# Optimization experiments

Measured on AMD Instinct MI355X. Metric: run time of the kernel, lower is better.

## Reference

```python
import jax, jax.numpy as jnp
import numpy as np

N_HEADS = 16
ROPE_BASE = 10000.0


def _rope_tables(T, head_dim):
    inv_freq = 1.0 / (ROPE_BASE ** (jnp.arange(0, head_dim, 2, dtype=jnp.float32) / head_dim))
    freqs = jnp.outer(jnp.arange(T, dtype=jnp.float32), inv_freq)  # (T, head_dim/2)
    emb = jnp.concatenate([freqs, freqs], axis=-1)  # (T, head_dim)
    return jnp.cos(emb), jnp.sin(emb)


def _rotate_half(u):
    u1, u2 = jnp.split(u, 2, axis=-1)
    return jnp.concatenate([-u2, u1], axis=-1)


def setup_inputs() -> dict:
    key = jax.random.key(0)
    k1, k2, k3 = jax.random.split(key, 3)
    B, T, D = 2, 2048, 1024
    x = jax.random.normal(k1, (B, T, D), dtype=jnp.float32)
    W_qkv = jax.random.normal(k2, (D, 3 * D), dtype=jnp.float32) * (1.0 / np.sqrt(D))
    W_out = jax.random.normal(k3, (D, D), dtype=jnp.float32) * (1.0 / np.sqrt(D))
    return {"x": x, "W_qkv": W_qkv, "W_out": W_out}


def reference(x, W_qkv, W_out):
    B, T, D = x.shape
    H = N_HEADS
    Dh = D // H
    # fused QKV projection
    qkv = (x @ W_qkv).reshape(B, T, 3, H, Dh)
    q = jnp.transpose(qkv[:, :, 0], (0, 2, 1, 3))  # (B,H,T,Dh)
    k = jnp.transpose(qkv[:, :, 1], (0, 2, 1, 3))
    v = jnp.transpose(qkv[:, :, 2], (0, 2, 1, 3))
    # RoPE
    cos, sin = _rope_tables(T, Dh)  # (T, Dh), broadcasts over (B,H)
    q = q * cos + _rotate_half(q) * sin
    k = k * cos + _rotate_half(k) * sin
    # causal SDPA
    scale = 1.0 / jnp.sqrt(jnp.asarray(Dh, dtype=x.dtype))
    scores = jnp.einsum('bhqd,bhkd->bhqk', q, k) * scale
    causal = jnp.tril(jnp.ones((T, T), dtype=bool))
    scores = jnp.where(causal, scores, jnp.asarray(-jnp.inf, dtype=scores.dtype))
    attn = jax.nn.softmax(scores, axis=-1)
    out = jnp.einsum('bhqk,bhkd->bhqd', attn, v)
    out = jnp.transpose(out, (0, 2, 1, 3)).reshape(B, T, D)
    return out @ W_out
```

## Files before the change

### kernel.cpp

```cpp
#include <hip/hip_runtime.h>
#include <math.h>

typedef unsigned short u16;
typedef short bf16x8 __attribute__((ext_vector_type(8)));
typedef float f32x4 __attribute__((ext_vector_type(4)));

#define ROPE_SC 0.18033688011112042f

__device__ __forceinline__ u16 f2bf(float f) {
    union { float f; unsigned u; } x; x.f = f;
    unsigned u = x.u;
    unsigned r = (u + 0x7fffu + ((u >> 16) & 1u)) >> 16;
    return (u16)r;
}
__device__ __forceinline__ unsigned pack2(float a, float b) {
    return (unsigned)f2bf(a) | ((unsigned)f2bf(b) << 16);
}
__device__ __forceinline__ f32x4 mfma16(bf16x8 a, bf16x8 b, f32x4 c) {
    return __builtin_amdgcn_mfma_f32_16x16x32_bf16(a, b, c, 0, 0, 0);
}
__device__ __forceinline__ void gload_lds16(const void* g, void* l) {
    __builtin_amdgcn_global_load_lds((const __attribute__((address_space(1))) void*)g,
                                     (__attribute__((address_space(3))) void*)l,
                                     16, 0, 0);
}

__global__ void cvt_bf16(const float* __restrict__ X, u16* __restrict__ Y) {
    int i = (blockIdx.x * 256 + threadIdx.x) * 4;
    float4 v = *(const float4*)(X + i);
    uint2 o;
    o.x = pack2(v.x, v.y);
    o.y = pack2(v.z, v.w);
    *(uint2*)(Y + i) = o;
}

__global__ void transpose_cvt(const float* __restrict__ W, u16* __restrict__ Wt,
                              int R, int C) {
    __shared__ u16 tile[32][33];
    int tx = threadIdx.x & 31, ty = threadIdx.x >> 5;
    int bx = blockIdx.x * 32;
    int by = blockIdx.y * 32;
#pragma unroll
    for (int r = ty; r < 32; r += 8)
        tile[r][tx] = f2bf(W[(size_t)(by + r) * C + bx + tx]);
    __syncthreads();
#pragma unroll
    for (int r = ty; r < 32; r += 8)
        Wt[(size_t)(bx + r) * R + by + tx] = tile[tx][r];
}

__global__ void rope_tab(float* __restrict__ tab) {
    int i = blockIdx.x * 256 + threadIdx.x;
    int t = i >> 5, d = i & 31;
    float invf = powf(10000.0f, -(float)d / 32.0f);
    float ang = (float)t * invf;
    tab[i] = cosf(ang);
    tab[i + 65536] = sinf(ang);
}

__global__ __launch_bounds__(256) void gemm_qkv(const u16* __restrict__ A,
                                                const u16* __restrict__ Bt,
                                                const float* __restrict__ tab,
                                                u16* __restrict__ qb,
                                                u16* __restrict__ kb,
                                                u16* __restrict__ vt,
                                                int M, int N, int K) {
    __shared__ u16 lA[128 * 64];
    __shared__ u16 lB[128 * 64];
    const int tid = threadIdx.x;
    const int wave = tid >> 6, lane = tid & 63;
    const int l15 = lane & 15, l4 = lane >> 4;
    const int nwg = gridDim.x * gridDim.y;
    const int orig = blockIdx.y * gridDim.x + blockIdx.x;
    const int swz = (orig & 7) * (nwg >> 3) + (orig >> 3);
    const int m0 = (swz / gridDim.x) * 128, n0 = (swz % gridDim.x) * 128;
    const int wm = (wave >> 1) * 64, wn = (wave & 1) * 64;
    f32x4 acc[4][4] = {};
    for (int k0 = 0; k0 < K; k0 += 64) {
#pragma unroll
        for (int it = 0; it < 4; ++it) {
            int c = it * 256 + wave * 64 + lane;
            int r = c >> 3, s = c & 7;
            int sd = ((s ^ (r & 7)) << 3);
            gload_lds16(A + (size_t)(m0 + r) * K + k0 + sd,
                        &lA[(size_t)(it * 256 + wave * 64) * 8]);
            gload_lds16(Bt + (size_t)(n0 + r) * K + k0 + sd,
                        &lB[(size_t)(it * 256 + wave * 64) * 8]);
        }
        __syncthreads();
#pragma unroll
        for (int kk = 0; kk < 2; ++kk) {
            bf16x8 af[4], bf[4];
#pragma unroll
            for (int mi = 0; mi < 4; ++mi) {
                int row = wm + mi * 16 + l15;
                af[mi] = *(const bf16x8*)(&lA[row * 64 + (((kk * 4 + l4) ^ (row & 7)) << 3)]);
            }
#pragma unroll
            for (int ni = 0; ni < 4; ++ni) {
                int row = wn + ni * 16 + l15;
                bf[ni] = *(const bf16x8*)(&lB[row * 64 + (((kk * 4 + l4) ^ (row & 7)) << 3)]);
            }
#pragma unroll
            for (int mi = 0; mi < 4; ++mi)
#pragma unroll
                for (int ni = 0; ni < 4; ++ni)
                    acc[mi][ni] = mfma16(af[mi], bf[ni], acc[mi][ni]);
        }
        __syncthreads();
    }
    const int colg = n0 + wn;
    const int region = colg >> 10;
    const int h = (colg & 1023) >> 6;
    if (region == 2) {
#pragma unroll
        for (int mi = 0; mi < 4; ++mi) {
            int t0 = m0 + wm + mi * 16 + l4 * 4;
            int b = t0 >> 11, tq0 = t0 & 2047;
#pragma unroll
            for (int ni = 0; ni < 4; ++ni) {
                int dcol = ni * 16 + l15;
                uint2 pk;
                pk.x = pack2(acc[mi][ni][0], acc[mi][ni][1]);
                pk.y = pack2(acc[mi][ni][2], acc[mi][ni][3]);
                *(uint2*)(vt + ((size_t)(b * 16 + h) * 64 + dcol) * 2048 + tq0) = pk;
            }
        }
    } else {
        const float sc = (region == 0) ? ROPE_SC : 1.0f;
        u16* dst = (region == 0) ? qb : kb;
#pragma unroll
        for (int mi = 0; mi < 4; ++mi)
#pragma unroll
            for (int i = 0; i < 4; ++i) {
                int t = m0 + wm + mi * 16 + l4 * 4 + i;
                int b = t >> 11, tq = t & 2047;
                const float* tcb = tab + tq * 32;
                const float* tsb = tab + 65536 + tq * 32;
                size_t base = ((size_t)(b * 16 + h) * 2048 + tq) * 64;
#pragma unroll
                for (int ni = 0; ni < 2; ++ni) {
                    int d32 = ni * 16 + l15;
                    float cs = tcb[d32], sn = tsb[d32];
                    float a = acc[mi][ni][i], bb = acc[mi][ni + 2][i];
                    dst[base + d32]      = f2bf((a * cs - bb * sn) * sc);
                    dst[base + d32 + 32] = f2bf((bb * cs + a * sn) * sc);
                }
            }
    }
}

__global__ __launch_bounds__(256) void gemm_bt_n64(const u16* __restrict__ A,
                                                   const u16* __restrict__ Bt,
                                                   float* __restrict__ C,
                                                   int M, int N, int K) {
    __shared__ u16 lA[128 * 64];
    __shared__ u16 lB[64 * 64];
    const int tid = threadIdx.x;
    const int wave = tid >> 6, lane = tid & 63;
    const int l15 = lane & 15, l4 = lane >> 4;
    const int nwg = gridDim.x * gridDim.y;
    const int orig = blockIdx.y * gridDim.x + blockIdx.x;
    const int swz = (orig & 7) * (nwg >> 3) + (orig >> 3);
    const int m0 = (swz / gridDim.x) * 128, n0 = (swz % gridDim.x) * 64;
    const int wm = (wave >> 1) * 64, wn = (wave & 1) * 32;
    f32x4 acc[4][2] = {};
    for (int k0 = 0; k0 < K; k0 += 64) {
#pragma unroll
        for (int it = 0; it < 4; ++it) {
            int c = it * 256 + wave * 64 + lane;
            int r = c >> 3, s = c & 7;
            int sd = ((s ^ (r & 7)) << 3);
            gload_lds16(A + (size_t)(m0 + r) * K + k0 + sd,
                        &lA[(size_t)(it * 256 + wave * 64) * 8]);
        }
#pragma unroll
        for (int it = 0; it < 2; ++it) {
            int c = it * 256 + wave * 64 + lane;
            int r = c >> 3, s = c & 7;
            int sd = ((s ^ (r & 7)) << 3);
            gload_lds16(Bt + (size_t)(n0 + r) * K + k0 + sd,
                        &lB[(size_t)(it * 256 + wave * 64) * 8]);
        }
        __syncthreads();
#pragma unroll
        for (int kk = 0; kk < 2; ++kk) {
            bf16x8 af[4], bf[2];
#pragma unroll
            for (int mi = 0; mi < 4; ++mi) {
                int row = wm + mi * 16 + l15;
                af[mi] = *(const bf16x8*)(&lA[row * 64 + (((kk * 4 + l4) ^ (row & 7)) << 3)]);
            }
#pragma unroll
            for (int ni = 0; ni < 2; ++ni) {
                int row = wn + ni * 16 + l15;
                bf[ni] = *(const bf16x8*)(&lB[row * 64 + (((kk * 4 + l4) ^ (row & 7)) << 3)]);
            }
#pragma unroll
            for (int mi = 0; mi < 4; ++mi)
#pragma unroll
                for (int ni = 0; ni < 2; ++ni)
                    acc[mi][ni] = mfma16(af[mi], bf[ni], acc[mi][ni]);
        }
        __syncthreads();
    }
#pragma unroll
    for (int mi = 0; mi < 4; ++mi)
#pragma unroll
        for (int ni = 0; ni < 2; ++ni)
#pragma unroll
            for (int i = 0; i < 4; ++i) {
                int r = m0 + wm + mi * 16 + l4 * 4 + i;
                int cc = n0 + wn + ni * 16 + l15;
                C[(size_t)r * N + cc] = acc[mi][ni][i];
            }
}

__global__ __launch_bounds__(256, 2) void flash11(const u16* __restrict__ qb,
                                                  const u16* __restrict__ kb,
                                                  const u16* __restrict__ vt,
                                                  u16* __restrict__ ao) {
    __shared__ u16 lK[2][64 * 64];
    __shared__ u16 lV[2][64 * 64];
    const int orig = blockIdx.x;
    const int xcd = orig & 7, p = orig >> 3;
    const int bh = xcd * 4 + (p & 3);
    const int j = (p < 32) ? ((p >> 2) & 7) : 15 - ((p >> 2) & 7);
    const int b = bh >> 4, h = bh & 15;
    const int tid = threadIdx.x;
    const int wave = tid >> 6, lane = tid & 63;
    const int l15 = lane & 15, l4 = lane >> 4;
    const int niter = 2 * (j + 1);
    const u16* qptr = qb + (size_t)bh * 2048 * 64;
    const u16* kptr = kb + (size_t)bh * 2048 * 64;
    const u16* vptr = vt + (size_t)bh * 64 * 2048;

    int qrow[2];
    bf16x8 q0[2], q1[2];
#pragma unroll
    for (int g = 0; g < 2; ++g) {
        qrow[g] = j * 128 + wave * 32 + g * 16 + l15;
        q0[g] = *(const bf16x8*)(qptr + (size_t)qrow[g] * 64 + l4 * 8);
        q1[g] = *(const bf16x8*)(qptr + (size_t)qrow[g] * 64 + 32 + l4 * 8);
    }

    f32x4 O[2][4] = {};
    float mrun[2] = { -INFINITY, -INFINITY }, lrun[2] = { 0.f, 0.f };

    int idxO[4];
#pragma unroll
    for (int i = 0; i < 4; ++i) idxO[i] = (lane & 48) | (l4 * 4 + i);

    const int r0q = ((l15 >> 2) << 3) | (l15 & 3);

    auto stage = [&](int buf, int kv0) {
#pragma unroll
        for (int it = 0; it < 2; ++it) {
            int cb = wave * 64 + it * 256;
            int c = cb + lane;
            int r = c >> 3, s = c & 7;
            int fK = (r & 3) | ((r >> 1) & 4);
            gload_lds16(kptr + (size_t)(kv0 + r) * 64 + ((s ^ fK) << 3), &lK[buf][cb * 8]);
            gload_lds16(vptr + (size_t)r * 2048 + kv0 + ((s ^ (r & 7)) << 3), &lV[buf][cb * 8]);
        }
    };
    auto ldK = [&](int buf, int row, int slot) -> bf16x8 {
        int f = (row & 3) | ((row >> 1) & 4);
        return *(const bf16x8*)(&lK[buf][row * 64 + ((slot ^ f) << 3)]);
    };
    auto ldV = [&](int buf, int row, int slot) -> bf16x8 {
        return *(const bf16x8*)(&lV[buf][row * 64 + ((slot ^ (row & 7)) << 3)]);
    };

    auto smpack = [&](f32x4 S[4], float& mr, float& lr, f32x4 Ov[4],
                      bf16x8 af[2], bool diag, int kv0, int qr) {
        float p2[4][4];
#pragma unroll
        for (int m = 0; m < 4; ++m)
#pragma unroll
            for (int i = 0; i < 4; ++i) {
                float s = S[m][i];
                if (diag && (kv0 + ((m >> 1) << 5) + (l4 << 3) + ((m & 1) << 2) + i > qr))
                    s = -INFINITY;
                p2[m][i] = s;
            }
        float m = p2[0][0];
#pragma unroll
        for (int c = 0; c < 4; ++c)
#pragma unroll
            for (int i = 0; i < 4; ++i) m = fmaxf(m, p2[c][i]);
        m = fmaxf(m, __shfl_xor(m, 16));
        m = fmaxf(m, __shfl_xor(m, 32));
        float mnew = fmaxf(mr, m);
        float corr = __builtin_amdgcn_exp2f(mr - mnew);
        float rs = 0.f;
#pragma unroll
        for (int c = 0; c < 4; ++c)
#pragma unroll
            for (int i = 0; i < 4; ++i) { p2[c][i] = __builtin_amdgcn_exp2f(p2[c][i] - mnew); rs += p2[c][i]; }
        rs += __shfl_xor(rs, 16);
        rs += __shfl_xor(rs, 32);
        lr = lr * corr + rs;
        mr = mnew;
#pragma unroll
        for (int i = 0; i < 4; ++i) {
            float cf = __shfl(corr, idxO[i]);
#pragma unroll
            for (int c2 = 0; c2 < 4; ++c2) Ov[c2][i] *= cf;
        }
        unsigned w[4][2];
#pragma unroll
        for (int c = 0; c < 4; ++c) {
            asm("v_cvt_pk_bf16_f32 %0, %1, %2" : "=v"(w[c][0]) : "v"(p2[c][0]), "v"(p2[c][1]));
            asm("v_cvt_pk_bf16_f32 %0, %1, %2" : "=v"(w[c][1]) : "v"(p2[c][2]), "v"(p2[c][3]));
        }
#pragma unroll
        for (int ks = 0; ks < 2; ++ks) {
            union { unsigned u[4]; bf16x8 v; } cvt;
            cvt.u[0] = w[2 * ks][0];
            cvt.u[1] = w[2 * ks][1];
            cvt.u[2] = w[2 * ks + 1][0];
            cvt.u[3] = w[2 * ks + 1][1];
            af[ks] = cvt.v;
        }
    };

    stage(0, 0);
    for (int kvb = 0; kvb < niter; ++kvb) {
        const int cur = kvb & 1;
        const int kv0 = kvb * 64;
        if (kvb < niter - 1) {
            stage(cur ^ 1, kv0 + 64);
            asm volatile("s_waitcnt vmcnt(4)" ::: "memory");
        } else {
            asm volatile("s_waitcnt vmcnt(0)" ::: "memory");
        }
        __builtin_amdgcn_s_barrier();
        __builtin_amdgcn_sched_barrier(0);

        f32x4 S0[4] = {}, S1[4] = {};
#pragma unroll
        for (int mm = 0; mm < 4; ++mm) {
            int row = r0q + ((mm >> 1) << 5) + ((mm & 1) << 2);
            bf16x8 kf0 = ldK(cur, row, l4);
            bf16x8 kf1 = ldK(cur, row, 4 + l4);
            S0[mm] = mfma16(kf0, q0[0], S0[mm]);
            S0[mm] = mfma16(kf1, q1[0], S0[mm]);
            S1[mm] = mfma16(kf0, q0[1], S1[mm]);
            S1[mm] = mfma16(kf1, q1[1], S1[mm]);
        }
        const bool diag = (kvb >= niter - 2);
        bf16x8 af0[2], af1[2];
        smpack(S0, mrun[0], lrun[0], O[0], af0, diag, kv0, qrow[0]);
        smpack(S1, mrun[1], lrun[1], O[1], af1, diag, kv0, qrow[1]);
#pragma unroll
        for (int ks = 0; ks < 2; ++ks)
#pragma unroll
            for (int c2 = 0; c2 < 4; ++c2) {
                bf16x8 vf = ldV(cur, c2 * 16 + l15, ks * 4 + l4);
                O[0][c2] = mfma16(af0[ks], vf, O[0][c2]);
                O[1][c2] = mfma16(af1[ks], vf, O[1][c2]);
            }
        __builtin_amdgcn_s_barrier();
    }

#pragma unroll
    for (int g = 0; g < 2; ++g)
#pragma unroll
        for (int i = 0; i < 4; ++i) {
            float lv = __shfl(lrun[g], idxO[i]);
            float rcp = 1.f / lv;
            int qg = j * 128 + wave * 32 + g * 16 + l4 * 4 + i;
#pragma unroll
            for (int c2 = 0; c2 < 4; ++c2)
                ao[(size_t)(b * 2048 + qg) * 1024 + h * 64 + c2 * 16 + l15] = f2bf(O[g][c2][i] * rcp);
        }
}

extern "C" void kernel_launch(void* const* d_in, const int* in_sizes, int n_in,
                              void* d_out, int out_size, void* d_ws, size_t ws_size,
                              hipStream_t stream) {
    const float* x    = (const float*)d_in[0];
    const float* Wqkv = (const float*)d_in[1];
    const float* Wout = (const float*)d_in[2];
    float* out = (float*)d_out;
    char* ws = (char*)d_ws;

    u16*   xb  = (u16*)(ws + 0);
    u16*   Wtq = (u16*)(ws + 8388608);
    u16*   Wto = (u16*)(ws + 14680064);
    u16*   qb  = (u16*)(ws + 67108864);
    u16*   kb  = (u16*)(ws + 75497472);
    u16*   vt  = (u16*)(ws + 83886080);
    float* tab = (float*)(ws + 92274688);
    u16*   ao  = (u16*)(ws + 0);

    cvt_bf16<<<dim3(4096), dim3(256), 0, stream>>>(x, xb);
    transpose_cvt<<<dim3(96, 32), dim3(256), 0, stream>>>(Wqkv, Wtq, 1024, 3072);
    transpose_cvt<<<dim3(32, 32), dim3(256), 0, stream>>>(Wout, Wto, 1024, 1024);
    rope_tab<<<dim3(256), dim3(256), 0, stream>>>(tab);
    gemm_qkv<<<dim3(24, 32), dim3(256), 0, stream>>>(xb, Wtq, tab, qb, kb, vt, 4096, 3072, 1024);
    flash11<<<dim3(512), dim3(256), 0, stream>>>(qb, kb, vt, ao);
    gemm_bt_n64<<<dim3(16, 32), dim3(256), 0, stream>>>(ao, Wto, out, 4096, 1024, 1024);
}
```

Before: 131.3 us.

## Use 8-wave GEMM blocks and 64-row flash tiles with more workgroups

Both GEMMs now launch 512 threads per block, with each wave owning half as many M rows. This raises wave-level parallelism and shrinks per-wave register footprint. The attention kernel goes back to 64-query-row tiles, one 16-row group per wave, and runs 1024 blocks with a new causal pairing schedule across XCDs and occupancy hint 4. The aim is better load balance and latency hiding, at the cost of less K/V reuse per block and more block overhead.

Result: faster. 110.8 us (-15.6%).

```diff
diff --git a/kernel.cpp b/kernel.cpp
--- a/kernel.cpp
+++ b/kernel.cpp
@@ -58,7 +58,7 @@
     tab[i + 65536] = sinf(ang);
 }
 
-__global__ __launch_bounds__(256) void gemm_qkv(const u16* __restrict__ A,
+__global__ __launch_bounds__(512) void gemm_qkv(const u16* __restrict__ A,
                                                 const u16* __restrict__ Bt,
                                                 const float* __restrict__ tab,
                                                 u16* __restrict__ qb,
@@ -74,25 +74,24 @@
     const int orig = blockIdx.y * gridDim.x + blockIdx.x;
     const int swz = (orig & 7) * (nwg >> 3) + (orig >> 3);
     const int m0 = (swz / gridDim.x) * 128, n0 = (swz % gridDim.x) * 128;
-    const int wm = (wave >> 1) * 64, wn = (wave & 1) * 64;
-    f32x4 acc[4][4] = {};
+    const int wm = (wave >> 1) * 32, wn = (wave & 1) * 64;
+    f32x4 acc[2][4] = {};
     for (int k0 = 0; k0 < K; k0 += 64) {
 #pragma unroll
-        for (int it = 0; it < 4; ++it) {
-            int c = it * 256 + wave * 64 + lane;
+        for (int it = 0; it < 2; ++it) {
+            int cb = it * 512 + wave * 64;
+            int c = cb + lane;
             int r = c >> 3, s = c & 7;
             int sd = ((s ^ (r & 7)) << 3);
-            gload_lds16(A + (size_t)(m0 + r) * K + k0 + sd,
-                        &lA[(size_t)(it * 256 + wave * 64) * 8]);
-            gload_lds16(Bt + (size_t)(n0 + r) * K + k0 + sd,
-                        &lB[(size_t)(it * 256 + wave * 64) * 8]);
+            gload_lds16(A + (size_t)(m0 + r) * K + k0 + sd, &lA[(size_t)cb * 8]);
+            gload_lds16(Bt + (size_t)(n0 + r) * K + k0 + sd, &lB[(size_t)cb * 8]);
         }
         __syncthreads();
 #pragma unroll
         for (int kk = 0; kk < 2; ++kk) {
-            bf16x8 af[4], bf[4];
-#pragma unroll
-            for (int mi = 0; mi < 4; ++mi) {
+            bf16x8 af[2], bf[4];
+#pragma unroll
+            for (int mi = 0; mi < 2; ++mi) {
                 int row = wm + mi * 16 + l15;
                 af[mi] = *(const bf16x8*)(&lA[row * 64 + (((kk * 4 + l4) ^ (row & 7)) << 3)]);
             }
@@ -102,7 +101,7 @@
                 bf[ni] = *(const bf16x8*)(&lB[row * 64 + (((kk * 4 + l4) ^ (row & 7)) << 3)]);
             }
 #pragma unroll
-            for (int mi = 0; mi < 4; ++mi)
+            for (int mi = 0; mi < 2; ++mi)
 #pragma unroll
                 for (int ni = 0; ni < 4; ++ni)
                     acc[mi][ni] = mfma16(af[mi], bf[ni], acc[mi][ni]);
@@ -114,7 +113,7 @@
     const int h = (colg & 1023) >> 6;
     if (region == 2) {
 #pragma unroll
-        for (int mi = 0; mi < 4; ++mi) {
+        for (int mi = 0; mi < 2; ++mi) {
             int t0 = m0 + wm + mi * 16 + l4 * 4;
             int b = t0 >> 11, tq0 = t0 & 2047;
 #pragma unroll
@@ -130,7 +129,7 @@
         const float sc = (region == 0) ? ROPE_SC : 1.0f;
         u16* dst = (region == 0) ? qb : kb;
 #pragma unroll
-        for (int mi = 0; mi < 4; ++mi)
+        for (int mi = 0; mi < 2; ++mi)
 #pragma unroll
             for (int i = 0; i < 4; ++i) {
                 int t = m0 + wm + mi * 16 + l4 * 4 + i;
@@ -150,7 +149,7 @@
     }
 }
 
-__global__ __launch_bounds__(256) void gemm_bt_n64(const u16* __restrict__ A,
+__global__ __launch_bounds__(512) void gemm_bt_n64(const u16* __restrict__ A,
                                                    const u16* __restrict__ Bt,
                                                    float* __restrict__ C,
                                                    int M, int N, int K) {
@@ -163,31 +162,30 @@
     const int orig = blockIdx.y * gridDim.x + blockIdx.x;
     const int swz = (orig & 7) * (nwg >> 3) + (orig >> 3);
     const int m0 = (swz / gridDim.x) * 128, n0 = (swz % gridDim.x) * 64;
-    const int wm = (wave >> 1) * 64, wn = (wave & 1) * 32;
-    f32x4 acc[4][2] = {};
+    const int wm = (wave >> 1) * 32, wn = (wave & 1) * 32;
+    f32x4 acc[2][2] = {};
     for (int k0 = 0; k0 < K; k0 += 64) {
 #pragma unroll
-        for (int it = 0; it < 4; ++it) {
-            int c = it * 256 + wave * 64 + lane;
+        for (int it = 0; it < 2; ++it) {
+            int cb = it * 512 + wave * 64;
+            int c = cb + lane;
             int r = c >> 3, s = c & 7;
             int sd = ((s ^ (r & 7)) << 3);
-            gload_lds16(A + (size_t)(m0 + r) * K + k0 + sd,
-                        &lA[(size_t)(it * 256 + wave * 64) * 8]);
-        }
-#pragma unroll
-        for (int it = 0; it < 2; ++it) {
-            int c = it * 256 + wave * 64 + lane;
+            gload_lds16(A + (size_t)(m0 + r) * K + k0 + sd, &lA[(size_t)cb * 8]);
+        }
+        {
+            int cb = wave * 64;
+            int c = cb + lane;
             int r = c >> 3, s = c & 7;
             int sd = ((s ^ (r & 7)) << 3);
-            gload_lds16(Bt + (size_t)(n0 + r) * K + k0 + sd,
-                        &lB[(size_t)(it * 256 + wave * 64) * 8]);
+            gload_lds16(Bt + (size_t)(n0 + r) * K + k0 + sd, &lB[(size_t)cb * 8]);
         }
         __syncthreads();
 #pragma unroll
         for (int kk = 0; kk < 2; ++kk) {
-            bf16x8 af[4], bf[2];
-#pragma unroll
-            for (int mi = 0; mi < 4; ++mi) {
+            bf16x8 af[2], bf[2];
+#pragma unroll
+            for (int mi = 0; mi < 2; ++mi) {
                 int row = wm + mi * 16 + l15;
                 af[mi] = *(const bf16x8*)(&lA[row * 64 + (((kk * 4 + l4) ^ (row & 7)) << 3)]);
             }
@@ -197,7 +195,7 @@
                 bf[ni] = *(const bf16x8*)(&lB[row * 64 + (((kk * 4 + l4) ^ (row & 7)) << 3)]);
             }
 #pragma unroll
-            for (int mi = 0; mi < 4; ++mi)
+            for (int mi = 0; mi < 2; ++mi)
 #pragma unroll
                 for (int ni = 0; ni < 2; ++ni)
                     acc[mi][ni] = mfma16(af[mi], bf[ni], acc[mi][ni]);
@@ -205,7 +203,7 @@
         __syncthreads();
     }
 #pragma unroll
-    for (int mi = 0; mi < 4; ++mi)
+    for (int mi = 0; mi < 2; ++mi)
 #pragma unroll
         for (int ni = 0; ni < 2; ++ni)
 #pragma unroll
@@ -216,7 +214,7 @@
             }
 }
 
-__global__ __launch_bounds__(256, 2) void flash11(const u16* __restrict__ qb,
+__global__ __launch_bounds__(256, 4) void flash10(const u16* __restrict__ qb,
                                                   const u16* __restrict__ kb,
                                                   const u16* __restrict__ vt,
                                                   u16* __restrict__ ao) {
@@ -224,28 +222,23 @@
     __shared__ u16 lV[2][64 * 64];
     const int orig = blockIdx.x;
     const int xcd = orig & 7, p = orig >> 3;
-    const int bh = xcd * 4 + (p & 3);
-    const int j = (p < 32) ? ((p >> 2) & 7) : 15 - ((p >> 2) & 7);
+    const int cup = p & 31, layer = p >> 5;
+    const int bh = xcd * 4 + layer;
+    const int qt = (layer & 1) ? cup : 31 - cup;
     const int b = bh >> 4, h = bh & 15;
     const int tid = threadIdx.x;
     const int wave = tid >> 6, lane = tid & 63;
     const int l15 = lane & 15, l4 = lane >> 4;
-    const int niter = 2 * (j + 1);
     const u16* qptr = qb + (size_t)bh * 2048 * 64;
     const u16* kptr = kb + (size_t)bh * 2048 * 64;
     const u16* vptr = vt + (size_t)bh * 64 * 2048;
 
-    int qrow[2];
-    bf16x8 q0[2], q1[2];
-#pragma unroll
-    for (int g = 0; g < 2; ++g) {
-        qrow[g] = j * 128 + wave * 32 + g * 16 + l15;
-        q0[g] = *(const bf16x8*)(qptr + (size_t)qrow[g] * 64 + l4 * 8);
-        q1[g] = *(const bf16x8*)(qptr + (size_t)qrow[g] * 64 + 32 + l4 * 8);
-    }
-
-    f32x4 O[2][4] = {};
-    float mrun[2] = { -INFINITY, -INFINITY }, lrun[2] = { 0.f, 0.f };
+    const int qrow = qt * 64 + wave * 16 + l15;
+    bf16x8 q0 = *(const bf16x8*)(qptr + (size_t)qrow * 64 + l4 * 8);
+    bf16x8 q1 = *(const bf16x8*)(qptr + (size_t)qrow * 64 + 32 + l4 * 8);
+
+    f32x4 O[4] = {};
+    float mrun = -INFINITY, lrun = 0.f;
 
     int idxO[4];
 #pragma unroll
@@ -326,10 +319,10 @@
     };
 
     stage(0, 0);
-    for (int kvb = 0; kvb < niter; ++kvb) {
+    for (int kvb = 0; kvb <= qt; ++kvb) {
         const int cur = kvb & 1;
         const int kv0 = kvb * 64;
-        if (kvb < niter - 1) {
+        if (kvb < qt) {
             stage(cur ^ 1, kv0 + 64);
             asm volatile("s_waitcnt vmcnt(4)" ::: "memory");
         } else {
@@ -338,43 +331,36 @@
         __builtin_amdgcn_s_barrier();
         __builtin_amdgcn_sched_barrier(0);
 
-        f32x4 S0[4] = {}, S1[4] = {};
+        f32x4 S[4] = {};
 #pragma unroll
         for (int mm = 0; mm < 4; ++mm) {
             int row = r0q + ((mm >> 1) << 5) + ((mm & 1) << 2);
             bf16x8 kf0 = ldK(cur, row, l4);
             bf16x8 kf1 = ldK(cur, row, 4 + l4);
-            S0[mm] = mfma16(kf0, q0[0], S0[mm]);
-            S0[mm] = mfma16(kf1, q1[0], S0[mm]);
-            S1[mm] = mfma16(kf0, q0[1], S1[mm]);
-            S1[mm] = mfma16(kf1, q1[1], S1[mm]);
-        }
-        const bool diag = (kvb >= niter - 2);
-        bf16x8 af0[2], af1[2];
-        smpack(S0, mrun[0], lrun[0], O[0], af0, diag, kv0, qrow[0]);
-        smpack(S1, mrun[1], lrun[1], O[1], af1, diag, kv0, qrow[1]);
+            S[mm] = mfma16(kf0, q0, S[mm]);
+            S[mm] = mfma16(kf1, q1, S[mm]);
+        }
+        bf16x8 af[2];
+        smpack(S, mrun, lrun, O, af, kvb == qt, kv0, qrow);
 #pragma unroll
         for (int ks = 0; ks < 2; ++ks)
 #pragma unroll
             for (int c2 = 0; c2 < 4; ++c2) {
                 bf16x8 vf = ldV(cur, c2 * 16 + l15, ks * 4 + l4);
-                O[0][c2] = mfma16(af0[ks], vf, O[0][c2]);
-                O[1][c2] = mfma16(af1[ks], vf, O[1][c2]);
+                O[c2] = mfma16(af[ks], vf, O[c2]);
             }
         __builtin_amdgcn_s_barrier();
     }
 
 #pragma unroll
-    for (int g = 0; g < 2; ++g)
-#pragma unroll
-        for (int i = 0; i < 4; ++i) {
-            float lv = __shfl(lrun[g], idxO[i]);
-            float rcp = 1.f / lv;
-            int qg = j * 128 + wave * 32 + g * 16 + l4 * 4 + i;
-#pragma unroll
-            for (int c2 = 0; c2 < 4; ++c2)
-                ao[(size_t)(b * 2048 + qg) * 1024 + h * 64 + c2 * 16 + l15] = f2bf(O[g][c2][i] * rcp);
-        }
+    for (int i = 0; i < 4; ++i) {
+        float lv = __shfl(lrun, idxO[i]);
+        float rcp = 1.f / lv;
+        int qg = qt * 64 + wave * 16 + l4 * 4 + i;
+#pragma unroll
+        for (int c2 = 0; c2 < 4; ++c2)
+            ao[(size_t)(b * 2048 + qg) * 1024 + h * 64 + c2 * 16 + l15] = f2bf(O[c2][i] * rcp);
+    }
 }
 
 extern "C" void kernel_launch(void* const* d_in, const int* in_sizes, int n_in,
@@ -399,7 +385,7 @@
     transpose_cvt<<<dim3(96, 32), dim3(256), 0, stream>>>(Wqkv, Wtq, 1024, 3072);
     transpose_cvt<<<dim3(32, 32), dim3(256), 0, stream>>>(Wout, Wto, 1024, 1024);
     rope_tab<<<dim3(256), dim3(256), 0, stream>>>(tab);
-    gemm_qkv<<<dim3(24, 32), dim3(256), 0, stream>>>(xb, Wtq, tab, qb, kb, vt, 4096, 3072, 1024);
-    flash11<<<dim3(512), dim3(256), 0, stream>>>(qb, kb, vt, ao);
-    gemm_bt_n64<<<dim3(16, 32), dim3(256), 0, stream>>>(ao, Wto, out, 4096, 1024, 1024);
-}
+    gemm_qkv<<<dim3(24, 32), dim3(512), 0, stream>>>(xb, Wtq, tab, qb, kb, vt, 4096, 3072, 1024);
+    flash10<<<dim3(1024), dim3(256), 0, stream>>>(qb, kb, vt, ao);
+    gemm_bt_n64<<<dim3(16, 32), dim3(512), 0, stream>>>(ao, Wto, out, 4096, 1024, 1024);
+}
```
